# Kernel tuning notes

Hardware: AMD Instinct MI355X
Metric: run time of the kernel (lower is better)

Reference implementation:

```python
import jax, jax.numpy as jnp
import numpy as np

NUM_HEADS = 32
HEAD_DIM = 128
ROPE_THETA = 10000.0


def _rope_tables(seq_len, head_dim, theta):
    inv_freq = 1.0 / (theta ** (jnp.arange(0, head_dim, 2, dtype=jnp.float32) / head_dim))
    pos = jnp.arange(seq_len, dtype=jnp.float32)
    freqs = pos[:, None] * inv_freq[None, :]            # [S, hd/2]
    emb = jnp.concatenate([freqs, freqs], axis=-1)      # [S, hd]
    return jnp.cos(emb), jnp.sin(emb)


def _rotate_half(x):
    x1, x2 = jnp.split(x, 2, axis=-1)
    return jnp.concatenate([-x2, x1], axis=-1)


def _apply_rope(x, cos, sin):
    # x: [B, S, H, D]; cos/sin: [S, D] -> unsqueeze_dim=2 broadcasting
    c = cos[None, :, None, :]
    s = sin[None, :, None, :]
    return x * c + _rotate_half(x) * s


def setup_inputs() -> dict:
    key = jax.random.key(0)
    ks = jax.random.split(key, 6)
    hidden = 4096
    B, S = 2, 4096  # global sequence = world_size * local_seq (4 * 1024)
    hidden_states = jax.random.normal(ks[0], (B, S, hidden), dtype=jnp.float32)
    # original uses torch.rand (uniform); scaled by 0.02 for numerical sanity
    q_proj = jax.random.uniform(ks[1], (hidden, hidden), dtype=jnp.float32) * 0.02
    k_proj = jax.random.uniform(ks[2], (hidden, hidden), dtype=jnp.float32) * 0.02
    v_proj = jax.random.uniform(ks[3], (hidden, hidden), dtype=jnp.float32) * 0.02
    o_proj = jax.random.uniform(ks[4], (hidden, hidden), dtype=jnp.float32) * 0.02
    return {"hidden_states": hidden_states, "q_proj": q_proj, "k_proj": k_proj,
            "v_proj": v_proj, "o_proj": o_proj, "world_size": 4}


def _ring_attention(hidden_states, q_proj, k_proj, v_proj, o_proj, world_size):
    B, S, H = hidden_states.shape
    s_local = S // world_size
    nh, hd = NUM_HEADS, HEAD_DIM
    scale = 1.0 / np.sqrt(hd).astype(np.float32)

    # rank 0 holds the first sequence shard as its local hidden states
    hs_local = hidden_states[:, :s_local]
    q = (hs_local @ q_proj.T).reshape(B, s_local, nh, hd)
    k = (hidden_states @ k_proj.T).reshape(B, S, nh, hd)
    v = (hidden_states @ v_proj.T).reshape(B, S, nh, hd)

    cos, sin = _rope_tables(S, hd, ROPE_THETA)
    q = _apply_rope(q, cos[:s_local], sin[:s_local])   # rank0 positions 0..s_local-1
    k = _apply_rope(k, cos, sin)                       # global positions per shard

    # split into per-rank KV blocks; rank 0 receives blocks W-1, W-2, ..., 0
    k_blocks = k.reshape(B, world_size, s_local, nh, hd).transpose(1, 0, 2, 3, 4)[::-1]
    v_blocks = v.reshape(B, world_size, s_local, nh, hd).transpose(1, 0, 2, 3, 4)[::-1]

    def step(carry, kv):
        attn, max_lse, denom, lse_full = carry
        k_blk, v_blk = kv
        # memory_efficient_attention_partial: non-causal partial attention + lse
        s = jnp.einsum('bqhd,bkhd->bhqk', q, k_blk) * scale
        m = jnp.max(s, axis=-1)                          # [B,H,q]
        p = jnp.exp(s - m[..., None])
        l = jnp.sum(p, axis=-1)
        lse = (m + jnp.log(l)).transpose(0, 2, 1)        # [B,q,H]
        out = jnp.einsum('bhqk,bkhd->bqhd', p / l[..., None], v_blk)
        # online-softmax merge across ring steps
        new_max = jnp.maximum(max_lse, lse)
        old_adj = jnp.exp(max_lse - new_max)[..., None]
        new_adj = jnp.exp(lse - new_max)[..., None]
        denom = old_adj * denom + new_adj
        attn = old_adj * attn + new_adj * out
        lse_full = new_max + jnp.log(jnp.exp(lse_full - new_max) + jnp.exp(lse - new_max))
        return (attn, new_max, denom, lse_full), None

    init = (jnp.zeros((B, s_local, nh, hd), jnp.float32),
            jnp.full((B, s_local, nh), -jnp.inf, jnp.float32),
            jnp.zeros((B, s_local, nh, 1), jnp.float32),
            jnp.full((B, s_local, nh), -jnp.inf, jnp.float32))
    (attn, _, denom, _), _ = jax.lax.scan(step, init, (k_blocks, v_blocks))

    attn = attn / denom
    attn = attn.astype(jnp.float16).astype(jnp.float32)  # .half() in source
    attn = attn.reshape(B, s_local, nh * hd)
    return attn @ o_proj.T


def reference(hidden_states, q_proj, k_proj, v_proj, o_proj, world_size):
    return _ring_attention(hidden_states, q_proj, k_proj, v_proj, o_proj, world_size)
```

## Files before the change

### kernel.cpp

```cpp
#include <hip/hip_runtime.h>


using bf16x8 = __attribute__((ext_vector_type(8))) short;
using f32x4  = __attribute__((ext_vector_type(4))) float;

__device__ inline unsigned short f32_to_bf16_bits(float f) {
  unsigned int u = __float_as_uint(f);
  u += 0x7FFFu + ((u >> 16) & 1u);
  return (unsigned short)(u >> 16);
}
__device__ inline float bf16_bits_to_f32(unsigned short h) {
  return __uint_as_float(((unsigned int)h) << 16);
}

__device__ __forceinline__ void load_lds16(const unsigned short* g, unsigned short* l) {
  __builtin_amdgcn_global_load_lds(
      (const __attribute__((address_space(1))) void*)g,
      (__attribute__((address_space(3))) void*)l, 16, 0, 0);
}

__global__ void cast_f32_bf16(const float* __restrict__ in,
                              unsigned short* __restrict__ out, long n4) {
  long i = (long)blockIdx.x * blockDim.x + threadIdx.x;
  long stride = (long)gridDim.x * blockDim.x;
  for (; i < n4; i += stride) {
    float4 v = reinterpret_cast<const float4*>(in)[i];
    ushort4 o;
    o.x = f32_to_bf16_bits(v.x);
    o.y = f32_to_bf16_bits(v.y);
    o.z = f32_to_bf16_bits(v.z);
    o.w = f32_to_bf16_bits(v.w);
    reinterpret_cast<ushort4*>(out)[i] = o;
  }
}

__global__ void rope_tables(float* __restrict__ cos_t, float* __restrict__ sin_t) {
  int idx = blockIdx.x * 256 + threadIdx.x;
  if (idx >= 4096 * 64) return;
  int p = idx >> 6, i = idx & 63;
  float inv = __expf(-(float)i * (9.210340371976184f / 64.0f));
  float f = (float)p * inv;
  cos_t[idx] = cosf(f);
  sin_t[idx] = sinf(f);
}

__global__ void rope_apply(unsigned short* __restrict__ buf,
                           const float* __restrict__ cos_t,
                           const float* __restrict__ sin_t,
                           long total, int pos_mask, float gain) {
  long idx = (long)blockIdx.x * 256 + threadIdx.x;
  if (idx >= total) return;
  long tok = idx >> 11;
  int rem  = (int)(idx & 2047);
  int head = rem >> 6, i = rem & 63;
  int pos  = (int)(tok & (long)pos_mask);
  float c = cos_t[pos * 64 + i], s = sin_t[pos * 64 + i];
  long base = tok * 4096 + head * 128 + i;
  float x1 = bf16_bits_to_f32(buf[base]);
  float x2 = bf16_bits_to_f32(buf[base + 64]);
  buf[base]      = f32_to_bf16_bits((x1 * c - x2 * s) * gain);
  buf[base + 64] = f32_to_bf16_bits((x2 * c + x1 * s) * gain);
}

__device__ inline void storeC(float* p, float v) { *p = v; }
__device__ inline void storeC(unsigned short* p, float v) { *p = f32_to_bf16_bits(v); }

template <typename OUT_T>
__global__ __launch_bounds__(256) void gemm_bt(const unsigned short* __restrict__ A,
                                               const unsigned short* __restrict__ B,
                                               OUT_T* __restrict__ C,
                                               long Astride_z, long Cstride_z, int N) {
  __shared__ unsigned short As[128 * 32];
  __shared__ unsigned short Bs[128 * 32];
  const int tid = threadIdx.x;
  const int bn = blockIdx.x, bm = blockIdx.y, bz = blockIdx.z;
  const unsigned short* Ab = A + (long)bz * Astride_z + (long)bm * 128 * 4096;
  const unsigned short* Bb = B + (long)bn * 128 * 4096;
  OUT_T* Cb = C + (long)bz * Cstride_z + (long)bm * 128 * N + (long)bn * 128;

  const int lane = tid & 63;
  const int w = tid >> 6;
  const int wr = (w >> 1) * 64, wc = (w & 1) * 64;
  const int fr = lane & 15, fg = lane >> 4;

  f32x4 acc[4][4] = {};

  const int c0 = tid, c1 = tid + 256;
  const int rA0 = c0 >> 2, kc0 = c0 & 3;
  const int rA1 = c1 >> 2, kc1 = c1 & 3;

  for (int k0 = 0; k0 < 4096; k0 += 32) {
    load_lds16(Ab + (long)rA0 * 4096 + k0 + kc0 * 8, As + c0 * 8);
    load_lds16(Ab + (long)rA1 * 4096 + k0 + kc1 * 8, As + c1 * 8);
    load_lds16(Bb + (long)rA0 * 4096 + k0 + kc0 * 8, Bs + c0 * 8);
    load_lds16(Bb + (long)rA1 * 4096 + k0 + kc1 * 8, Bs + c1 * 8);
    __syncthreads();
    bf16x8 af[4], bfv[4];
#pragma unroll
    for (int m = 0; m < 4; m++)
      af[m] = *reinterpret_cast<const bf16x8*>(As + (wr + m * 16 + fr) * 32 + fg * 8);
#pragma unroll
    for (int n = 0; n < 4; n++)
      bfv[n] = *reinterpret_cast<const bf16x8*>(Bs + (wc + n * 16 + fr) * 32 + fg * 8);
#pragma unroll
    for (int m = 0; m < 4; m++)
#pragma unroll
      for (int n = 0; n < 4; n++)
        acc[m][n] = __builtin_amdgcn_mfma_f32_16x16x32_bf16(af[m], bfv[n], acc[m][n], 0, 0, 0);
    __syncthreads();
  }
#pragma unroll
  for (int m = 0; m < 4; m++)
#pragma unroll
    for (int n = 0; n < 4; n++)
#pragma unroll
      for (int r = 0; r < 4; r++) {
        int row = wr + m * 16 + fg * 4 + r;
        int col = wc + n * 16 + fr;
        storeC(Cb + (long)row * N + col, acc[m][n][r]);
      }
}


#define STG2(Gb, Lb, h, kc)                                                    \
  load_lds16((Gb) + (long)((h) * 128 + srow) * 4096 + sslot * 8 + (kc),        \
             (Lb) + tid * 8);                                                  \
  load_lds16((Gb) + (long)((h) * 128 + 64 + srow) * 4096 + sslot * 8 + (kc),   \
             (Lb) + 4096 + tid * 8);

#define MFMAQ(MH, NH)                                                          \
  _Pragma("unroll") for (int mi = 0; mi < 4; ++mi)                             \
    _Pragma("unroll") for (int ni = 0; ni < 2; ++ni)                           \
      _Pragma("unroll") for (int kk = 0; kk < 2; ++kk)                         \
        acc[(MH) * 4 + mi][(NH) * 2 + ni] =                                    \
            __builtin_amdgcn_mfma_f32_16x16x32_bf16(                           \
                a[mi][kk], b[(NH) * 2 + ni][kk],                               \
                acc[(MH) * 4 + mi][(NH) * 2 + ni], 0, 0, 0);

#define TILE(P, KC, MODE)                                                      \
  {                                                                            \
    const unsigned short* Ar = lds + wm * 16384 + (P) * 8192;                  \
    const unsigned short* Br =                                                 \
        lds + 32768 + (wn >> 1) * 16384 + (P) * 8192 + (wn & 1) * 4096;        \
    _Pragma("unroll") for (int mf = 0; mf < 4; ++mf) {                         \
      a[mf][0] = *reinterpret_cast<const bf16x8*>(Ar + mf * 1024 + ao0);       \
      a[mf][1] = *reinterpret_cast<const bf16x8*>(Ar + mf * 1024 + ao1);       \
    }                                                                          \
    _Pragma("unroll") for (int nf = 0; nf < 2; ++nf) {                         \
      b[nf][0] = *reinterpret_cast<const bf16x8*>(Br + nf * 1024 + ao0);       \
      b[nf][1] = *reinterpret_cast<const bf16x8*>(Br + nf * 1024 + ao1);       \
    }                                                                          \
    __builtin_amdgcn_s_setprio(1);                                             \
    MFMAQ(0, 0);                                                               \
    __builtin_amdgcn_s_setprio(0);                                             \
    _Pragma("unroll") for (int nf = 2; nf < 4; ++nf) {                         \
      b[nf][0] = *reinterpret_cast<const bf16x8*>(Br + nf * 1024 + ao0);       \
      b[nf][1] = *reinterpret_cast<const bf16x8*>(Br + nf * 1024 + ao1);       \
    }                                                                          \
    __builtin_amdgcn_s_setprio(1);                                             \
    MFMAQ(0, 1);                                                               \
    __builtin_amdgcn_s_setprio(0);                                             \
    asm volatile("s_waitcnt lgkmcnt(0)" ::: "memory");                         \
    asm volatile("s_barrier" ::: "memory");            \
    if ((MODE) == 0) {                                                         \
      STG2(Bg, lds + 32768 + (P) * 8192, 0, KC);                               \
      STG2(Bg, lds + 49152 + (P) * 8192, 1, KC);                               \
    }                                                                          \
    _Pragma("unroll") for (int mf = 0; mf < 4; ++mf) {                         \
      a[mf][0] = *reinterpret_cast<const bf16x8*>(Ar + (4 + mf) * 1024 + ao0); \
      a[mf][1] = *reinterpret_cast<const bf16x8*>(Ar + (4 + mf) * 1024 + ao1); \
    }                                                                          \
    __builtin_amdgcn_s_setprio(1);                                             \
    MFMAQ(1, 0);                                                               \
    __builtin_amdgcn_s_setprio(0);                                             \
    asm volatile("s_waitcnt lgkmcnt(0)" ::: "memory");                         \
    asm volatile("s_barrier" ::: "memory");            \
    if ((MODE) == 0) {                                                         \
      STG2(Ag, lds + (P) * 8192, 0, KC);                                       \
      STG2(Ag, lds + 16384 + (P) * 8192, 1, KC);                               \
    }                                                                          \
    __builtin_amdgcn_s_setprio(1);                                             \
    MFMAQ(1, 1);                                                               \
    __builtin_amdgcn_s_setprio(0);                                             \
    if ((MODE) == 0) asm volatile("s_waitcnt vmcnt(8)" ::: "memory");          \
    if ((MODE) == 1) asm volatile("s_waitcnt vmcnt(0)" ::: "memory");          \
    asm volatile("s_barrier" ::: "memory");       \
  }

template <typename OUT_T>
__global__ __launch_bounds__(512, 2) void gemm256(const unsigned short* __restrict__ A,
                                                  const unsigned short* __restrict__ B,
                                                  OUT_T* __restrict__ C,
                                                  long Astride_z, long Cstride_z, int N) {
  __shared__ unsigned short lds[65536];
  const int tid = threadIdx.x;
  const int bn = blockIdx.x, bm = blockIdx.y, bz = blockIdx.z;
  const unsigned short* Ag = A + (long)bz * Astride_z + (long)bm * 256 * 4096;
  const unsigned short* Bg = B + (long)bn * 256 * 4096;

  const int w = tid >> 6, lane = tid & 63;
  const int wm = w >> 2, wn = w & 3;
  const int fr = lane & 15, fg = lane >> 4;
  const int ao0 = fr * 64 + ((fg ^ (fr & 7)) * 8);
  const int ao1 = fr * 64 + (((4 + fg) ^ (fr & 7)) * 8);
  const int srow = tid >> 3;
  const int sslot = (tid & 7) ^ (srow & 7);

  f32x4 acc[8][4] = {};
  bf16x8 a[4][2], b[4][2];

  STG2(Ag, lds + 0, 0, 0);     STG2(Ag, lds + 16384, 1, 0);
  STG2(Bg, lds + 32768, 0, 0); STG2(Bg, lds + 49152, 1, 0);
  STG2(Ag, lds + 8192, 0, 64);  STG2(Ag, lds + 24576, 1, 64);
  STG2(Bg, lds + 40960, 0, 64); STG2(Bg, lds + 57344, 1, 64);
  asm volatile("s_waitcnt vmcnt(8)" ::: "memory");
  asm volatile("s_barrier" ::: "memory");

  for (int ti = 0; ti < 31; ++ti) {
    TILE(0, (2 * ti + 2) * 64, 0);
    TILE(1, (2 * ti + 3) * 64, 0);
  }
  TILE(0, 0, 1);
  TILE(1, 0, 2);

  OUT_T* Cb = C + (long)bz * Cstride_z + ((long)bm * 256) * N + bn * 256;
#pragma unroll
  for (int mf = 0; mf < 8; ++mf)
#pragma unroll
    for (int nf = 0; nf < 4; ++nf)
#pragma unroll
      for (int rr = 0; rr < 4; ++rr) {
        int row = wm * 128 + mf * 16 + fg * 4 + rr;
        int col = wn * 64 + nf * 16 + fr;
        storeC(Cb + (long)row * N + col, acc[mf][nf][rr]);
      }
}

__global__ __launch_bounds__(256) void attn_fwd(const unsigned short* __restrict__ qb,
                                                const unsigned short* __restrict__ kb,
                                                const unsigned short* __restrict__ vT,
                                                unsigned short* __restrict__ ob) {
  __shared__ unsigned short Ks[64 * 128];
  __shared__ unsigned short Vl[128 * 64];
  __shared__ unsigned short Ps[4][16 * 72];

  const int qt = blockIdx.x, h = blockIdx.y, b = blockIdx.z;
  const int tid = threadIdx.x, w = tid >> 6, lane = tid & 63;
  const int fr = lane & 15, fg = lane >> 4;

  const unsigned short* kbase = kb + (long)b * 4096 * 4096 + h * 128;
  const unsigned short* vbase = vT + (long)h * 128 * 8192 + (long)b * 4096;

  bf16x8 qf[4];
  {
    const unsigned short* qptr =
        qb + ((long)b * 1024 + qt * 64 + w * 16 + fr) * 4096 + h * 128 + fg * 8;
#pragma unroll
    for (int c = 0; c < 4; c++) qf[c] = *reinterpret_cast<const bf16x8*>(qptr + c * 32);
  }

  f32x4 outa[8] = {};
  float m_run[4], l_run[4];
#pragma unroll
  for (int r = 0; r < 4; r++) { m_run[r] = -1e30f; l_run[r] = 0.0f; }

  for (int kv0 = 0; kv0 < 4096; kv0 += 64) {
    __syncthreads();
#pragma unroll
    for (int i = 0; i < 4; i++) {
      int c = tid + 256 * i;
      int key = c >> 4, s = c & 15;
      int Lg = s ^ (key & 15);
      load_lds16(kbase + (long)(kv0 + key) * 4096 + Lg * 8, Ks + c * 8);
    }
#pragma unroll
    for (int i = 0; i < 4; i++) {
      int c = tid + 256 * i;
      int f = c >> 3, s = c & 7;
      int Lg = s ^ (f & 7);
      load_lds16(vbase + (long)f * 8192 + kv0 + Lg * 8, Vl + c * 8);
    }
    __syncthreads();

    f32x4 sacc[4];
#pragma unroll
    for (int ks = 0; ks < 4; ks++) {
      f32x4 aq = {0.f, 0.f, 0.f, 0.f};
#pragma unroll
      for (int cc = 0; cc < 4; cc++) {
        bf16x8 kf = *reinterpret_cast<const bf16x8*>(
            &Ks[(ks * 16 + fr) * 128 + (((cc * 4 + fg) ^ fr) & 15) * 8]);
        aq = __builtin_amdgcn_mfma_f32_16x16x32_bf16(qf[cc], kf, aq, 0, 0, 0);
      }
      sacc[ks] = aq;
    }

    float mx4[4];
#pragma unroll
    for (int r = 0; r < 4; r++) {
      float mx = fmaxf(fmaxf(sacc[0][r], sacc[1][r]), fmaxf(sacc[2][r], sacc[3][r]));
      mx = fmaxf(mx, __shfl_xor(mx, 1));
      mx = fmaxf(mx, __shfl_xor(mx, 2));
      mx = fmaxf(mx, __shfl_xor(mx, 4));
      mx = fmaxf(mx, __shfl_xor(mx, 8));
      mx4[r] = mx;
    }
    int need = 0;
#pragma unroll
    for (int r = 0; r < 4; r++) need |= (mx4[r] > m_run[r] + 11.5f) ? 1 : 0;
    if (__any(need)) {
#pragma unroll
      for (int r = 0; r < 4; r++) {
        float mnew = fmaxf(m_run[r], mx4[r]);
        float ef = exp2f(m_run[r] - mnew);
        l_run[r] *= ef;
        m_run[r] = mnew;
#pragma unroll
        for (int ds = 0; ds < 8; ds++) outa[ds][r] *= ef;
      }
    }
    float p[4][4];
#pragma unroll
    for (int r = 0; r < 4; r++) {
      float sum = 0.f;
#pragma unroll
      for (int ks = 0; ks < 4; ks++) {
        float pv = exp2f(sacc[ks][r] - m_run[r]);
        p[ks][r] = pv;
        sum += pv;
      }
      sum += __shfl_xor(sum, 1);
      sum += __shfl_xor(sum, 2);
      sum += __shfl_xor(sum, 4);
      sum += __shfl_xor(sum, 8);
      l_run[r] += sum;
    }

#pragma unroll
    for (int r = 0; r < 4; r++)
#pragma unroll
      for (int ks = 0; ks < 4; ks++)
        Ps[w][(fg * 4 + r) * 72 + ks * 16 + fr] = f32_to_bf16_bits(p[ks][r]);

#pragma unroll
    for (int c2 = 0; c2 < 2; c2++) {
      bf16x8 pf = *reinterpret_cast<const bf16x8*>(&Ps[w][fr * 72 + c2 * 32 + fg * 8]);
#pragma unroll
      for (int ds = 0; ds < 8; ds++) {
        int feat = ds * 16 + fr;
        int pch = ((c2 * 4 + fg) ^ (feat & 7)) & 7;
        bf16x8 vf = *reinterpret_cast<const bf16x8*>(&Vl[feat * 64 + pch * 8]);
        outa[ds] = __builtin_amdgcn_mfma_f32_16x16x32_bf16(pf, vf, outa[ds], 0, 0, 0);
      }
    }
  }

#pragma unroll
  for (int r = 0; r < 4; r++) {
    float inv = 1.0f / l_run[r];
    unsigned short* op =
        ob + ((long)b * 1024 + qt * 64 + w * 16 + fg * 4 + r) * 4096 + h * 128;
#pragma unroll
    for (int ds = 0; ds < 8; ds++) op[ds * 16 + fr] = f32_to_bf16_bits(outa[ds][r] * inv);
  }
}

extern "C" void kernel_launch(void* const* d_in, const int* in_sizes, int n_in,
                              void* d_out, int out_size, void* d_ws, size_t ws_size,
                              hipStream_t stream) {
  const float* hs = (const float*)d_in[0];
  const float* wq = (const float*)d_in[1];
  const float* wk = (const float*)d_in[2];
  const float* wv = (const float*)d_in[3];
  const float* wo = (const float*)d_in[4];
  float* out = (float*)d_out;

  const long hsN = 2L * 4096 * 4096;
  const long wN  = 4096L * 4096;

  unsigned short* hs_b = (unsigned short*)d_ws;
  unsigned short* wq_b = hs_b + hsN;
  unsigned short* wk_b = wq_b + wN;
  unsigned short* wv_b = wk_b + wN;
  unsigned short* wo_b = wv_b + wN;
  unsigned short* q_b  = wo_b + wN;
  unsigned short* k_b  = q_b + 2048L * 4096;
  unsigned short* vT_b = k_b + 8192L * 4096;
  unsigned short* at_b = vT_b + 8192L * 4096;
  float* cos_t = (float*)(at_b + 2048L * 4096);
  float* sin_t = cos_t + 4096 * 64;

  cast_f32_bf16<<<dim3(4096), dim3(256), 0, stream>>>(hs, hs_b, hsN / 4);
  cast_f32_bf16<<<dim3(2048), dim3(256), 0, stream>>>(wq, wq_b, wN / 4);
  cast_f32_bf16<<<dim3(2048), dim3(256), 0, stream>>>(wk, wk_b, wN / 4);
  cast_f32_bf16<<<dim3(2048), dim3(256), 0, stream>>>(wv, wv_b, wN / 4);
  cast_f32_bf16<<<dim3(2048), dim3(256), 0, stream>>>(wo, wo_b, wN / 4);

  rope_tables<<<dim3(1024), dim3(256), 0, stream>>>(cos_t, sin_t);

  gemm_bt<unsigned short><<<dim3(32, 8, 2), dim3(256), 0, stream>>>(
      hs_b, wq_b, q_b, 4096L * 4096, 1024L * 4096, 4096);
  gemm256<unsigned short><<<dim3(16, 16, 2), dim3(512), 0, stream>>>(
      hs_b, wk_b, k_b, 4096L * 4096, 4096L * 4096, 4096);
  gemm256<unsigned short><<<dim3(32, 16, 1), dim3(512), 0, stream>>>(
      wv_b, hs_b, vT_b, 0L, 0L, 8192);

  const float qgain = 0.08838834764831845f * 1.4426950408889634f;
  rope_apply<<<dim3(16384), dim3(256), 0, stream>>>(q_b, cos_t, sin_t, 2048L * 2048, 1023, qgain);
  rope_apply<<<dim3(65536), dim3(256), 0, stream>>>(k_b, cos_t, sin_t, 8192L * 2048, 4095, 1.0f);

  attn_fwd<<<dim3(16, 32, 2), dim3(256), 0, stream>>>(q_b, k_b, vT_b, at_b);

  gemm_bt<float><<<dim3(32, 16, 1), dim3(256), 0, stream>>>(
      at_b, wo_b, out, 0L, 0L, 4096);
}
```

Measured before the change: 1.124 ms.

## Process two query tiles per wave in attention and vectorize RoPE apply

Each attention wave now handles 32 query rows (two 16-row fragments), so every K and V fragment read from LDS is reused across two MFMA chains, and the grid is halved to 128-row query blocks. The per-row sum reduction across lanes is deferred from each KV step to the final normalization. RoPE application is rewritten to process 8 elements per thread with 16-byte vector loads and stores. The costs are higher register pressure from doubled accumulators and softmax state, which may lower occupancy, and fewer attention blocks in flight (512).

```diff
diff --git a/kernel.cpp b/kernel.cpp
--- a/kernel.cpp
+++ b/kernel.cpp
@@ -44,22 +44,35 @@
   sin_t[idx] = sinf(f);
 }
 
-__global__ void rope_apply(unsigned short* __restrict__ buf,
-                           const float* __restrict__ cos_t,
-                           const float* __restrict__ sin_t,
-                           long total, int pos_mask, float gain) {
+__global__ void rope_apply_v(unsigned short* __restrict__ buf,
+                             const float4* __restrict__ cos4,
+                             const float4* __restrict__ sin4,
+                             long nchunks, int pos_mask, float gain) {
   long idx = (long)blockIdx.x * 256 + threadIdx.x;
-  if (idx >= total) return;
-  long tok = idx >> 11;
-  int rem  = (int)(idx & 2047);
-  int head = rem >> 6, i = rem & 63;
-  int pos  = (int)(tok & (long)pos_mask);
-  float c = cos_t[pos * 64 + i], s = sin_t[pos * 64 + i];
-  long base = tok * 4096 + head * 128 + i;
-  float x1 = bf16_bits_to_f32(buf[base]);
-  float x2 = bf16_bits_to_f32(buf[base + 64]);
-  buf[base]      = f32_to_bf16_bits((x1 * c - x2 * s) * gain);
-  buf[base + 64] = f32_to_bf16_bits((x2 * c + x1 * s) * gain);
+  if (idx >= nchunks) return;
+  long tok = idx >> 8;
+  int rem = (int)(idx & 255);
+  int head = rem >> 3, c = rem & 7;
+  int pos = (int)(tok & (long)pos_mask);
+  float4 ct0 = cos4[pos * 16 + c * 2];
+  float4 ct1 = cos4[pos * 16 + c * 2 + 1];
+  float4 st0 = sin4[pos * 16 + c * 2];
+  float4 st1 = sin4[pos * 16 + c * 2 + 1];
+  float cs[8] = {ct0.x, ct0.y, ct0.z, ct0.w, ct1.x, ct1.y, ct1.z, ct1.w};
+  float sn[8] = {st0.x, st0.y, st0.z, st0.w, st1.x, st1.y, st1.z, st1.w};
+  long base = tok * 4096 + head * 128 + c * 8;
+  bf16x8 x1 = *reinterpret_cast<const bf16x8*>(buf + base);
+  bf16x8 x2 = *reinterpret_cast<const bf16x8*>(buf + base + 64);
+  bf16x8 o1, o2;
+#pragma unroll
+  for (int j = 0; j < 8; j++) {
+    float a = bf16_bits_to_f32((unsigned short)x1[j]);
+    float b = bf16_bits_to_f32((unsigned short)x2[j]);
+    o1[j] = (short)f32_to_bf16_bits((a * cs[j] - b * sn[j]) * gain);
+    o2[j] = (short)f32_to_bf16_bits((b * cs[j] + a * sn[j]) * gain);
+  }
+  *reinterpret_cast<bf16x8*>(buf + base) = o1;
+  *reinterpret_cast<bf16x8*>(buf + base + 64) = o2;
 }
 
 __device__ inline void storeC(float* p, float v) { *p = v; }
@@ -121,7 +134,6 @@
       }
 }
 
-
 #define STG2(Gb, Lb, h, kc)                                                    \
   load_lds16((Gb) + (long)((h) * 128 + srow) * 4096 + sslot * 8 + (kc),        \
              (Lb) + tid * 8);                                                  \
@@ -242,7 +254,7 @@
                                                 unsigned short* __restrict__ ob) {
   __shared__ unsigned short Ks[64 * 128];
   __shared__ unsigned short Vl[128 * 64];
-  __shared__ unsigned short Ps[4][16 * 72];
+  __shared__ unsigned short Ps[4][32 * 72];
 
   const int qt = blockIdx.x, h = blockIdx.y, b = blockIdx.z;
   const int tid = threadIdx.x, w = tid >> 6, lane = tid & 63;
@@ -251,18 +263,21 @@
   const unsigned short* kbase = kb + (long)b * 4096 * 4096 + h * 128;
   const unsigned short* vbase = vT + (long)h * 128 * 8192 + (long)b * 4096;
 
-  bf16x8 qf[4];
-  {
+  bf16x8 qf[2][4];
+#pragma unroll
+  for (int qi = 0; qi < 2; qi++) {
     const unsigned short* qptr =
-        qb + ((long)b * 1024 + qt * 64 + w * 16 + fr) * 4096 + h * 128 + fg * 8;
-#pragma unroll
-    for (int c = 0; c < 4; c++) qf[c] = *reinterpret_cast<const bf16x8*>(qptr + c * 32);
-  }
-
-  f32x4 outa[8] = {};
-  float m_run[4], l_run[4];
-#pragma unroll
-  for (int r = 0; r < 4; r++) { m_run[r] = -1e30f; l_run[r] = 0.0f; }
+        qb + ((long)b * 1024 + qt * 128 + w * 32 + qi * 16 + fr) * 4096 + h * 128 + fg * 8;
+#pragma unroll
+    for (int c = 0; c < 4; c++) qf[qi][c] = *reinterpret_cast<const bf16x8*>(qptr + c * 32);
+  }
+
+  f32x4 outa[2][8] = {};
+  float m_run[2][4], l_run[2][4];
+#pragma unroll
+  for (int qi = 0; qi < 2; qi++)
+#pragma unroll
+    for (int r = 0; r < 4; r++) { m_run[qi][r] = -1e30f; l_run[qi][r] = 0.0f; }
 
   for (int kv0 = 0; kv0 < 4096; kv0 += 64) {
     __syncthreads();
@@ -282,87 +297,101 @@
     }
     __syncthreads();
 
-    f32x4 sacc[4];
+    f32x4 sacc[2][4];
 #pragma unroll
     for (int ks = 0; ks < 4; ks++) {
-      f32x4 aq = {0.f, 0.f, 0.f, 0.f};
-#pragma unroll
-      for (int cc = 0; cc < 4; cc++) {
-        bf16x8 kf = *reinterpret_cast<const bf16x8*>(
+      bf16x8 kf[4];
+#pragma unroll
+      for (int cc = 0; cc < 4; cc++)
+        kf[cc] = *reinterpret_cast<const bf16x8*>(
             &Ks[(ks * 16 + fr) * 128 + (((cc * 4 + fg) ^ fr) & 15) * 8]);
-        aq = __builtin_amdgcn_mfma_f32_16x16x32_bf16(qf[cc], kf, aq, 0, 0, 0);
-      }
-      sacc[ks] = aq;
-    }
-
-    float mx4[4];
-#pragma unroll
-    for (int r = 0; r < 4; r++) {
-      float mx = fmaxf(fmaxf(sacc[0][r], sacc[1][r]), fmaxf(sacc[2][r], sacc[3][r]));
-      mx = fmaxf(mx, __shfl_xor(mx, 1));
-      mx = fmaxf(mx, __shfl_xor(mx, 2));
-      mx = fmaxf(mx, __shfl_xor(mx, 4));
-      mx = fmaxf(mx, __shfl_xor(mx, 8));
-      mx4[r] = mx;
-    }
+#pragma unroll
+      for (int qi = 0; qi < 2; qi++) {
+        f32x4 aq = {0.f, 0.f, 0.f, 0.f};
+#pragma unroll
+        for (int cc = 0; cc < 4; cc++)
+          aq = __builtin_amdgcn_mfma_f32_16x16x32_bf16(qf[qi][cc], kf[cc], aq, 0, 0, 0);
+        sacc[qi][ks] = aq;
+      }
+    }
+
+    float mx4[2][4];
+#pragma unroll
+    for (int qi = 0; qi < 2; qi++)
+#pragma unroll
+      for (int r = 0; r < 4; r++) {
+        float mx = fmaxf(fmaxf(sacc[qi][0][r], sacc[qi][1][r]),
+                         fmaxf(sacc[qi][2][r], sacc[qi][3][r]));
+        mx = fmaxf(mx, __shfl_xor(mx, 1));
+        mx = fmaxf(mx, __shfl_xor(mx, 2));
+        mx = fmaxf(mx, __shfl_xor(mx, 4));
+        mx = fmaxf(mx, __shfl_xor(mx, 8));
+        mx4[qi][r] = mx;
+      }
     int need = 0;
 #pragma unroll
-    for (int r = 0; r < 4; r++) need |= (mx4[r] > m_run[r] + 11.5f) ? 1 : 0;
+    for (int qi = 0; qi < 2; qi++)
+#pragma unroll
+      for (int r = 0; r < 4; r++)
+        need |= (mx4[qi][r] > m_run[qi][r] + 11.5f) ? 1 : 0;
     if (__any(need)) {
 #pragma unroll
+      for (int qi = 0; qi < 2; qi++)
+#pragma unroll
+        for (int r = 0; r < 4; r++) {
+          float mnew = fmaxf(m_run[qi][r], mx4[qi][r]);
+          float ef = exp2f(m_run[qi][r] - mnew);
+          l_run[qi][r] *= ef;
+          m_run[qi][r] = mnew;
+#pragma unroll
+          for (int ds = 0; ds < 8; ds++) outa[qi][ds][r] *= ef;
+        }
+    }
+#pragma unroll
+    for (int qi = 0; qi < 2; qi++)
+#pragma unroll
       for (int r = 0; r < 4; r++) {
-        float mnew = fmaxf(m_run[r], mx4[r]);
-        float ef = exp2f(m_run[r] - mnew);
-        l_run[r] *= ef;
-        m_run[r] = mnew;
-#pragma unroll
-        for (int ds = 0; ds < 8; ds++) outa[ds][r] *= ef;
-      }
-    }
-    float p[4][4];
-#pragma unroll
-    for (int r = 0; r < 4; r++) {
-      float sum = 0.f;
-#pragma unroll
-      for (int ks = 0; ks < 4; ks++) {
-        float pv = exp2f(sacc[ks][r] - m_run[r]);
-        p[ks][r] = pv;
-        sum += pv;
-      }
-      sum += __shfl_xor(sum, 1);
-      sum += __shfl_xor(sum, 2);
-      sum += __shfl_xor(sum, 4);
-      sum += __shfl_xor(sum, 8);
-      l_run[r] += sum;
-    }
-
-#pragma unroll
-    for (int r = 0; r < 4; r++)
-#pragma unroll
-      for (int ks = 0; ks < 4; ks++)
-        Ps[w][(fg * 4 + r) * 72 + ks * 16 + fr] = f32_to_bf16_bits(p[ks][r]);
+        float sum = 0.f;
+#pragma unroll
+        for (int ks = 0; ks < 4; ks++) {
+          float pv = exp2f(sacc[qi][ks][r] - m_run[qi][r]);
+          Ps[w][(qi * 16 + fg * 4 + r) * 72 + ks * 16 + fr] = f32_to_bf16_bits(pv);
+          sum += pv;
+        }
+        l_run[qi][r] += sum;
+      }
 
 #pragma unroll
     for (int c2 = 0; c2 < 2; c2++) {
-      bf16x8 pf = *reinterpret_cast<const bf16x8*>(&Ps[w][fr * 72 + c2 * 32 + fg * 8]);
+      bf16x8 pf0 = *reinterpret_cast<const bf16x8*>(&Ps[w][fr * 72 + c2 * 32 + fg * 8]);
+      bf16x8 pf1 = *reinterpret_cast<const bf16x8*>(&Ps[w][(16 + fr) * 72 + c2 * 32 + fg * 8]);
 #pragma unroll
       for (int ds = 0; ds < 8; ds++) {
         int feat = ds * 16 + fr;
         int pch = ((c2 * 4 + fg) ^ (feat & 7)) & 7;
         bf16x8 vf = *reinterpret_cast<const bf16x8*>(&Vl[feat * 64 + pch * 8]);
-        outa[ds] = __builtin_amdgcn_mfma_f32_16x16x32_bf16(pf, vf, outa[ds], 0, 0, 0);
-      }
-    }
-  }
-
-#pragma unroll
-  for (int r = 0; r < 4; r++) {
-    float inv = 1.0f / l_run[r];
-    unsigned short* op =
-        ob + ((long)b * 1024 + qt * 64 + w * 16 + fg * 4 + r) * 4096 + h * 128;
-#pragma unroll
-    for (int ds = 0; ds < 8; ds++) op[ds * 16 + fr] = f32_to_bf16_bits(outa[ds][r] * inv);
-  }
+        outa[0][ds] = __builtin_amdgcn_mfma_f32_16x16x32_bf16(pf0, vf, outa[0][ds], 0, 0, 0);
+        outa[1][ds] = __builtin_amdgcn_mfma_f32_16x16x32_bf16(pf1, vf, outa[1][ds], 0, 0, 0);
+      }
+    }
+  }
+
+#pragma unroll
+  for (int qi = 0; qi < 2; qi++)
+#pragma unroll
+    for (int r = 0; r < 4; r++) {
+      float l = l_run[qi][r];
+      l += __shfl_xor(l, 1);
+      l += __shfl_xor(l, 2);
+      l += __shfl_xor(l, 4);
+      l += __shfl_xor(l, 8);
+      float inv = 1.0f / l;
+      unsigned short* op =
+          ob + ((long)b * 1024 + qt * 128 + w * 32 + qi * 16 + fg * 4 + r) * 4096 + h * 128;
+#pragma unroll
+      for (int ds = 0; ds < 8; ds++)
+        op[ds * 16 + fr] = f32_to_bf16_bits(outa[qi][ds][r] * inv);
+    }
 }
 
 extern "C" void kernel_launch(void* const* d_in, const int* in_sizes, int n_in,
@@ -406,10 +435,12 @@
       wv_b, hs_b, vT_b, 0L, 0L, 8192);
 
   const float qgain = 0.08838834764831845f * 1.4426950408889634f;
-  rope_apply<<<dim3(16384), dim3(256), 0, stream>>>(q_b, cos_t, sin_t, 2048L * 2048, 1023, qgain);
-  rope_apply<<<dim3(65536), dim3(256), 0, stream>>>(k_b, cos_t, sin_t, 8192L * 2048, 4095, 1.0f);
-
-  attn_fwd<<<dim3(16, 32, 2), dim3(256), 0, stream>>>(q_b, k_b, vT_b, at_b);
+  rope_apply_v<<<dim3(2048), dim3(256), 0, stream>>>(
+      q_b, (const float4*)cos_t, (const float4*)sin_t, 2048L * 256, 1023, qgain);
+  rope_apply_v<<<dim3(8192), dim3(256), 0, stream>>>(
+      k_b, (const float4*)cos_t, (const float4*)sin_t, 8192L * 256, 4095, 1.0f);
+
+  attn_fwd<<<dim3(8, 32, 2), dim3(256), 0, stream>>>(q_b, k_b, vT_b, at_b);
 
   gemm_bt<float><<<dim3(32, 16, 1), dim3(256), 0, stream>>>(
       at_b, wo_b, out, 0L, 0L, 4096);
```

Result: no change. 1.141 ms (+1.4%).

## Double-buffer K/V tiles in attention, defer row-sum reduction, vectorize RoPE

Applied to the files above, without the earlier changes.

The attention kernel now keeps two LDS buffers for K and V. It issues async global-to-LDS loads for the next tile while computing the current one, so there is one barrier per iteration instead of two serialized load phases. The per-iteration cross-lane shuffle reduction of softmax row sums is moved to the end, since the partial sums add linearly under rescaling. RoPE application is vectorized to process 8 bf16 elements per thread with float4 table loads. The cost is doubled LDS use in attention, which may lower occupancy.

```diff
diff --git a/kernel.cpp b/kernel.cpp
--- a/kernel.cpp
+++ b/kernel.cpp
@@ -44,22 +44,35 @@
   sin_t[idx] = sinf(f);
 }
 
-__global__ void rope_apply(unsigned short* __restrict__ buf,
-                           const float* __restrict__ cos_t,
-                           const float* __restrict__ sin_t,
-                           long total, int pos_mask, float gain) {
+__global__ void rope_apply_v(unsigned short* __restrict__ buf,
+                             const float4* __restrict__ cos4,
+                             const float4* __restrict__ sin4,
+                             long nchunks, int pos_mask, float gain) {
   long idx = (long)blockIdx.x * 256 + threadIdx.x;
-  if (idx >= total) return;
-  long tok = idx >> 11;
-  int rem  = (int)(idx & 2047);
-  int head = rem >> 6, i = rem & 63;
-  int pos  = (int)(tok & (long)pos_mask);
-  float c = cos_t[pos * 64 + i], s = sin_t[pos * 64 + i];
-  long base = tok * 4096 + head * 128 + i;
-  float x1 = bf16_bits_to_f32(buf[base]);
-  float x2 = bf16_bits_to_f32(buf[base + 64]);
-  buf[base]      = f32_to_bf16_bits((x1 * c - x2 * s) * gain);
-  buf[base + 64] = f32_to_bf16_bits((x2 * c + x1 * s) * gain);
+  if (idx >= nchunks) return;
+  long tok = idx >> 8;
+  int rem = (int)(idx & 255);
+  int head = rem >> 3, c = rem & 7;
+  int pos = (int)(tok & (long)pos_mask);
+  float4 ct0 = cos4[pos * 16 + c * 2];
+  float4 ct1 = cos4[pos * 16 + c * 2 + 1];
+  float4 st0 = sin4[pos * 16 + c * 2];
+  float4 st1 = sin4[pos * 16 + c * 2 + 1];
+  float cs[8] = {ct0.x, ct0.y, ct0.z, ct0.w, ct1.x, ct1.y, ct1.z, ct1.w};
+  float sn[8] = {st0.x, st0.y, st0.z, st0.w, st1.x, st1.y, st1.z, st1.w};
+  long base = tok * 4096 + head * 128 + c * 8;
+  bf16x8 x1 = *reinterpret_cast<const bf16x8*>(buf + base);
+  bf16x8 x2 = *reinterpret_cast<const bf16x8*>(buf + base + 64);
+  bf16x8 o1, o2;
+#pragma unroll
+  for (int j = 0; j < 8; j++) {
+    float a = bf16_bits_to_f32((unsigned short)x1[j]);
+    float b = bf16_bits_to_f32((unsigned short)x2[j]);
+    o1[j] = (short)f32_to_bf16_bits((a * cs[j] - b * sn[j]) * gain);
+    o2[j] = (short)f32_to_bf16_bits((b * cs[j] + a * sn[j]) * gain);
+  }
+  *reinterpret_cast<bf16x8*>(buf + base) = o1;
+  *reinterpret_cast<bf16x8*>(buf + base + 64) = o2;
 }
 
 __device__ inline void storeC(float* p, float v) { *p = v; }
@@ -121,7 +134,6 @@
       }
 }
 
-
 #define STG2(Gb, Lb, h, kc)                                                    \
   load_lds16((Gb) + (long)((h) * 128 + srow) * 4096 + sslot * 8 + (kc),        \
              (Lb) + tid * 8);                                                  \
@@ -236,12 +248,26 @@
       }
 }
 
+#define AT_STAGE(P, kv)                                                        \
+  _Pragma("unroll") for (int i = 0; i < 4; i++) {                              \
+    int c = tid + 256 * i;                                                     \
+    int key = c >> 4, s0 = c & 15;                                             \
+    int Lg = s0 ^ (key & 15);                                                  \
+    load_lds16(kbase + (long)((kv) + key) * 4096 + Lg * 8, &Ks[P][c * 8]);     \
+  }                                                                            \
+  _Pragma("unroll") for (int i = 0; i < 4; i++) {                              \
+    int c = tid + 256 * i;                                                     \
+    int f0 = c >> 3, s0 = c & 7;                                               \
+    int Lg = s0 ^ (f0 & 7);                                                    \
+    load_lds16(vbase + (long)f0 * 8192 + (kv) + Lg * 8, &Vl[P][c * 8]);        \
+  }
+
 __global__ __launch_bounds__(256) void attn_fwd(const unsigned short* __restrict__ qb,
                                                 const unsigned short* __restrict__ kb,
                                                 const unsigned short* __restrict__ vT,
                                                 unsigned short* __restrict__ ob) {
-  __shared__ unsigned short Ks[64 * 128];
-  __shared__ unsigned short Vl[128 * 64];
+  __shared__ unsigned short Ks[2][64 * 128];
+  __shared__ unsigned short Vl[2][128 * 64];
   __shared__ unsigned short Ps[4][16 * 72];
 
   const int qt = blockIdx.x, h = blockIdx.y, b = blockIdx.z;
@@ -264,23 +290,13 @@
 #pragma unroll
   for (int r = 0; r < 4; r++) { m_run[r] = -1e30f; l_run[r] = 0.0f; }
 
-  for (int kv0 = 0; kv0 < 4096; kv0 += 64) {
-    __syncthreads();
-#pragma unroll
-    for (int i = 0; i < 4; i++) {
-      int c = tid + 256 * i;
-      int key = c >> 4, s = c & 15;
-      int Lg = s ^ (key & 15);
-      load_lds16(kbase + (long)(kv0 + key) * 4096 + Lg * 8, Ks + c * 8);
-    }
-#pragma unroll
-    for (int i = 0; i < 4; i++) {
-      int c = tid + 256 * i;
-      int f = c >> 3, s = c & 7;
-      int Lg = s ^ (f & 7);
-      load_lds16(vbase + (long)f * 8192 + kv0 + Lg * 8, Vl + c * 8);
-    }
-    __syncthreads();
+  AT_STAGE(0, 0);
+  asm volatile("s_waitcnt vmcnt(0)" ::: "memory");
+  asm volatile("s_barrier" ::: "memory");
+
+  for (int t = 0; t < 64; ++t) {
+    const int cur = t & 1;
+    if (t < 63) { AT_STAGE(cur ^ 1, (t + 1) * 64); }
 
     f32x4 sacc[4];
 #pragma unroll
@@ -289,7 +305,7 @@
 #pragma unroll
       for (int cc = 0; cc < 4; cc++) {
         bf16x8 kf = *reinterpret_cast<const bf16x8*>(
-            &Ks[(ks * 16 + fr) * 128 + (((cc * 4 + fg) ^ fr) & 15) * 8]);
+            &Ks[cur][(ks * 16 + fr) * 128 + (((cc * 4 + fg) ^ fr) & 15) * 8]);
         aq = __builtin_amdgcn_mfma_f32_16x16x32_bf16(qf[cc], kf, aq, 0, 0, 0);
       }
       sacc[ks] = aq;
@@ -319,28 +335,17 @@
         for (int ds = 0; ds < 8; ds++) outa[ds][r] *= ef;
       }
     }
-    float p[4][4];
 #pragma unroll
     for (int r = 0; r < 4; r++) {
       float sum = 0.f;
 #pragma unroll
       for (int ks = 0; ks < 4; ks++) {
         float pv = exp2f(sacc[ks][r] - m_run[r]);
-        p[ks][r] = pv;
+        Ps[w][(fg * 4 + r) * 72 + ks * 16 + fr] = f32_to_bf16_bits(pv);
         sum += pv;
       }
-      sum += __shfl_xor(sum, 1);
-      sum += __shfl_xor(sum, 2);
-      sum += __shfl_xor(sum, 4);
-      sum += __shfl_xor(sum, 8);
       l_run[r] += sum;
     }
-
-#pragma unroll
-    for (int r = 0; r < 4; r++)
-#pragma unroll
-      for (int ks = 0; ks < 4; ks++)
-        Ps[w][(fg * 4 + r) * 72 + ks * 16 + fr] = f32_to_bf16_bits(p[ks][r]);
 
 #pragma unroll
     for (int c2 = 0; c2 < 2; c2++) {
@@ -349,15 +354,26 @@
       for (int ds = 0; ds < 8; ds++) {
         int feat = ds * 16 + fr;
         int pch = ((c2 * 4 + fg) ^ (feat & 7)) & 7;
-        bf16x8 vf = *reinterpret_cast<const bf16x8*>(&Vl[feat * 64 + pch * 8]);
+        bf16x8 vf = *reinterpret_cast<const bf16x8*>(&Vl[cur][feat * 64 + pch * 8]);
         outa[ds] = __builtin_amdgcn_mfma_f32_16x16x32_bf16(pf, vf, outa[ds], 0, 0, 0);
       }
     }
+
+    if (t < 63) {
+      asm volatile("s_waitcnt lgkmcnt(0)" ::: "memory");
+      asm volatile("s_waitcnt vmcnt(0)" ::: "memory");
+      asm volatile("s_barrier" ::: "memory");
+    }
   }
 
 #pragma unroll
   for (int r = 0; r < 4; r++) {
-    float inv = 1.0f / l_run[r];
+    float l = l_run[r];
+    l += __shfl_xor(l, 1);
+    l += __shfl_xor(l, 2);
+    l += __shfl_xor(l, 4);
+    l += __shfl_xor(l, 8);
+    float inv = 1.0f / l;
     unsigned short* op =
         ob + ((long)b * 1024 + qt * 64 + w * 16 + fg * 4 + r) * 4096 + h * 128;
 #pragma unroll
@@ -406,8 +422,10 @@
       wv_b, hs_b, vT_b, 0L, 0L, 8192);
 
   const float qgain = 0.08838834764831845f * 1.4426950408889634f;
-  rope_apply<<<dim3(16384), dim3(256), 0, stream>>>(q_b, cos_t, sin_t, 2048L * 2048, 1023, qgain);
-  rope_apply<<<dim3(65536), dim3(256), 0, stream>>>(k_b, cos_t, sin_t, 8192L * 2048, 4095, 1.0f);
+  rope_apply_v<<<dim3(2048), dim3(256), 0, stream>>>(
+      q_b, (const float4*)cos_t, (const float4*)sin_t, 2048L * 256, 1023, qgain);
+  rope_apply_v<<<dim3(8192), dim3(256), 0, stream>>>(
+      k_b, (const float4*)cos_t, (const float4*)sin_t, 8192L * 256, 4095, 1.0f);
 
   attn_fwd<<<dim3(16, 32, 2), dim3(256), 0, stream>>>(q_b, k_b, vT_b, at_b);
 
```

Measured after the change: 1.078 ms. 4.1% less time.
